# Optimization experiments

Measured on AMD Instinct MI355X. Metric: run time of the kernel, lower is better.

Reference implementation:

```python
import jax, jax.numpy as jnp
import numpy as np
from jax import lax

IMAGENET_MEAN = jnp.array([0.485, 0.456, 0.406], dtype=jnp.float32).reshape(1, 3, 1, 1)
IMAGENET_STD = jnp.array([0.229, 0.224, 0.225], dtype=jnp.float32).reshape(1, 3, 1, 1)
MAX_ITERS = 10
TEMPERATURE = 500.0


def conv3x3(x, w, b):
    # NCHW conv, stride 1, padding 1 (same as nn.Conv2d(k=3, padding=1))
    y = lax.conv_general_dilated(x, w, (1, 1), ((1, 1), (1, 1)),
                                 dimension_numbers=("NCHW", "OIHW", "NCHW"))
    return y + b[None, :, None, None]


def setup_inputs() -> dict:
    key = jax.random.key(0)
    k = jax.random.split(key, 8)
    B, H, W = 8, 512, 512
    real_img = jax.random.uniform(k[0], (B, 3, H, W), dtype=jnp.float32)
    pred_img = jax.random.uniform(k[1], (B, 3, H, W), dtype=jnp.float32)
    mask = jax.random.uniform(k[2], (B, 1, H, W), dtype=jnp.float32)
    # VGG19 first two convs (random-init stand-ins, scaled like kaiming-ish)
    w1 = jax.random.normal(k[3], (64, 3, 3, 3), dtype=jnp.float32) * 0.1
    b1 = jax.random.normal(k[4], (64,), dtype=jnp.float32) * 0.01
    w2 = jax.random.normal(k[5], (64, 64, 3, 3), dtype=jnp.float32) * 0.05
    b2 = jax.random.normal(k[6], (64,), dtype=jnp.float32) * 0.01
    erode_w = jnp.ones((1, 1, 3, 3), dtype=jnp.float32)  # weight.data.fill_(1)
    return {"real_img": real_img, "pred_img": pred_img, "mask": mask,
            "w1": w1, "b1": b1, "w2": w2, "b2": b2, "erode_w": erode_w}


def _forward(real_img, pred_img, mask, w1, b1, w2, b2, erode_w):
    x = (real_img - IMAGENET_MEAN) / IMAGENET_STD
    # features = conv1_1 -> relu -> conv1_2 -> relu (level=2, no pooling reached)
    f = jax.nn.relu(conv3x3(x, w1, b1))
    real_feats = jax.nn.relu(conv3x3(f, w2, b2))  # [B,64,H,W]

    dv = real_feats[:, :, 1:, :] - real_feats[:, :, :-1, :]
    vertical_sim = jnp.exp(-jnp.sum(dv * dv, axis=1, keepdims=True) / TEMPERATURE)  # [B,1,H-1,W]
    dh = real_feats[:, :, :, 1:] - real_feats[:, :, :, :-1]
    horizontal_sim = jnp.exp(-jnp.sum(dh * dh, axis=1, keepdims=True) / TEMPERATURE)  # [B,1,H,W-1]

    B, _, Hf, Wf = real_feats.shape
    # bilinear resize, half-pixel centers == F.interpolate(align_corners=False)
    mask_scaled = jax.image.resize(mask, (B, 1, Hf, Wf), method="bilinear")
    # erode: all-ones 3x3 conv (zero pad), threshold > 1
    eroded = lax.conv_general_dilated(mask_scaled, erode_w, (1, 1), ((1, 1), (1, 1)),
                                      dimension_numbers=("NCHW", "OIHW", "NCHW"))
    mask_scaled = (eroded > 1.0).astype(jnp.float32)

    cur0 = 1.0 - mask_scaled

    def body(i, cur):
        top = cur[:, :, :-1, :] * vertical_sim
        new_top = jnp.concatenate([top[:, :, :1, :], top], axis=2)  # replicate pad top
        bot = cur[:, :, 1:, :] * vertical_sim
        new_bot = jnp.concatenate([bot, bot[:, :, -1:, :]], axis=2)  # replicate pad bottom
        lef = cur[:, :, :, :-1] * horizontal_sim
        new_lef = jnp.concatenate([lef[:, :, :, :1], lef], axis=3)  # replicate pad left
        rig = cur[:, :, :, 1:] * horizontal_sim
        new_rig = jnp.concatenate([rig, rig[:, :, :, -1:]], axis=3)  # replicate pad right
        new_know = jnp.maximum(jnp.maximum(new_top, new_bot), jnp.maximum(new_lef, new_rig))
        return jnp.maximum(cur, new_know)

    cur_knowness = lax.fori_loop(0, MAX_ITERS, body, cur0)

    Hm, Wm = mask.shape[-2:]
    cur_knowness = jax.image.resize(cur_knowness, (B, 1, Hm, Wm), method="bilinear")
    return jnp.minimum(mask, 1.0 - cur_knowness)


def reference(real_img, pred_img, mask, w1, b1, w2, b2, erode_w):
    return _forward(real_img, pred_img, mask, w1, b1, w2, b2, erode_w)
```

## Files before the change

kernel.cpp:

```cpp
#include <hip/hip_runtime.h>
#include <hip/hip_bf16.h>

#define HH 512
#define WW 512
#define NB 8
#define IMG (HH*WW)
#define TS 15
#define NTL 35

typedef __bf16 bf16x8 __attribute__((ext_vector_type(8)));
typedef float  f32x4  __attribute__((ext_vector_type(4)));

__device__ __forceinline__ float bflo(unsigned u){ return __uint_as_float(u << 16); }
__device__ __forceinline__ float bfhi(unsigned u){ return __uint_as_float(u & 0xffff0000u); }
__device__ __forceinline__ unsigned f2bf_bits(float f){
    union { float f; unsigned u; } v; v.f = f;
    return (v.u + 0x7fffu + ((v.u >> 16) & 1u)) >> 16;
}
__device__ __forceinline__ unsigned packbf(float lo, float hi){
    return f2bf_bits(lo) | (f2bf_bits(hi) << 16);
}

__global__ void prep_kernel(const float* __restrict__ w2, const float* __restrict__ w1,
                            uint4* __restrict__ wb, uint4* __restrict__ wa)
{
    int i = blockIdx.x * 256 + threadIdx.x;
    if (i < 9*2*4*64){
        int tap = i >> 9;
        int rem = i & 511;
        int ks  = rem >> 8;
        int nf  = (rem >> 6) & 3;
        int l   = rem & 63;
        int oc  = nf*16 + (l & 15);
        int icb = ks*32 + (l >> 4)*8;
        float v[8];
        #pragma unroll
        for (int j = 0; j < 8; ++j)
            v[j] = w2[(oc*64 + icb + j)*9 + tap];
        uint4 q;
        q.x = packbf(v[0], v[1]); q.y = packbf(v[2], v[3]);
        q.z = packbf(v[4], v[5]); q.w = packbf(v[6], v[7]);
        wb[i] = q;
    } else if (i < 9*2*4*64 + 4*64){
        int idx = i - 9*2*4*64;
        int mf = idx >> 6, l = idx & 63;
        int oc = mf*16 + (l & 15);
        int kb = (l >> 4)*8;
        float v[8];
        #pragma unroll
        for (int j = 0; j < 8; ++j)
            v[j] = (kb + j < 27) ? w1[oc*27 + kb + j] : 0.f;
        uint4 q;
        q.x = packbf(v[0], v[1]); q.y = packbf(v[2], v[3]);
        q.z = packbf(v[4], v[5]); q.w = packbf(v[6], v[7]);
        wa[idx] = q;
    }
}

__global__ void erode_init_kernel(const float* __restrict__ mask, float* __restrict__ cur)
{
    int idx = blockIdx.x * 256 + threadIdx.x;
    int b = idx >> 18, r = idx & (IMG - 1);
    int h = r >> 9, w = r & 511;
    const float* mb = mask + b*IMG;
    float s = 0.f;
    #pragma unroll
    for (int dy = -1; dy <= 1; ++dy){
        int hh = h + dy;
        if (hh < 0 || hh >= HH) continue;
        #pragma unroll
        for (int dx = -1; dx <= 1; ++dx){
            int ww = w + dx;
            if (ww < 0 || ww >= WW) continue;
            s += mb[hh*WW + ww];
        }
    }
    cur[idx] = (s > 1.0f) ? 0.f : 1.f;
}

__global__ __launch_bounds__(256, 2)
void conv_sims_kernel(const float* __restrict__ img,
                      const float* __restrict__ b1,
                      const uint4* __restrict__ wa,
                      const uint4* __restrict__ wb, const float* __restrict__ b2,
                      float* __restrict__ vs, float* __restrict__ hs)
{
    __shared__ float xs[3][20][20];
    __shared__ uint4 fs4[324*8];
    __shared__ uint4 uni[2048];

    const int tid = threadIdx.x;
    const int bid = blockIdx.x;
    const int b   = bid / (NTL*NTL);
    const int t2  = bid % (NTL*NTL);
    const int th  = t2 / NTL, tw = t2 % NTL;
    const int h0  = th * TS, w0 = tw * TS;

    for (int i = tid; i < 3*20*20; i += 256){
        int ic = i / 400, r = (i / 20) % 20, c = i % 20;
        int gy = h0 - 2 + r, gx = w0 - 2 + c;
        float mean = (ic == 0) ? 0.485f : (ic == 1) ? 0.456f : 0.406f;
        float istd = (ic == 0) ? (1.f/0.229f) : (ic == 1) ? (1.f/0.224f) : (1.f/0.225f);
        float v = 0.f;
        if (gy >= 0 && gy < HH && gx >= 0 && gx < WW)
            v = (img[(b*3 + ic)*IMG + gy*WW + gx] - mean) * istd;
        xs[ic][r][c] = v;
    }
    __syncthreads();

    {
        uint4* xi = uni;
        for (int p = tid; p < 336; p += 256){
            uint4 c0 = {0,0,0,0}, c1 = c0, c2 = c0, c3 = c0;
            if (p < 324){
                int fy = p / 18, fx = p % 18;
                float xv[27];
                #pragma unroll
                for (int ic = 0; ic < 3; ++ic)
                    #pragma unroll
                    for (int ky = 0; ky < 3; ++ky)
                        #pragma unroll
                        for (int kx = 0; kx < 3; ++kx)
                            xv[ic*9 + ky*3 + kx] = xs[ic][fy + ky][fx + kx];
                c0.x = packbf(xv[0], xv[1]);  c0.y = packbf(xv[2], xv[3]);
                c0.z = packbf(xv[4], xv[5]);  c0.w = packbf(xv[6], xv[7]);
                c1.x = packbf(xv[8], xv[9]);  c1.y = packbf(xv[10], xv[11]);
                c1.z = packbf(xv[12], xv[13]);c1.w = packbf(xv[14], xv[15]);
                c2.x = packbf(xv[16], xv[17]);c2.y = packbf(xv[18], xv[19]);
                c2.z = packbf(xv[20], xv[21]);c2.w = packbf(xv[22], xv[23]);
                c3.x = packbf(xv[24], xv[25]);c3.y = packbf(xv[26], 0.f);
            }
            int sw = p & 3;
            xi[p*4 + (0 ^ sw)] = c0;
            xi[p*4 + (1 ^ sw)] = c1;
            xi[p*4 + (2 ^ sw)] = c2;
            xi[p*4 + (3 ^ sw)] = c3;
        }
    }
    __syncthreads();

    {
        const int l  = tid & 63, wv = tid >> 6;
        const int lr = l & 15,  kg = l >> 4;
        const bf16x8* wav = (const bf16x8*)wa;
        const bf16x8* xib = (const bf16x8*)uni;

        bf16x8 af[4];
        #pragma unroll
        for (int mf = 0; mf < 4; ++mf) af[mf] = wav[(mf << 6) + l];
        f32x4 binit[4];
        #pragma unroll
        for (int mf = 0; mf < 4; ++mf)
            binit[mf] = *(const f32x4*)(b1 + mf*16 + kg*4);

        for (int nb = wv; nb < 21; nb += 4){
            int px = nb*16 + lr;
            bf16x8 bf = xib[px*4 + (kg ^ (px & 3))];
            int fy = px / 18, fx = px % 18;
            int gy = h0 - 1 + fy, gx = w0 - 1 + fx;
            bool inimg = (px < 324) && gy >= 0 && gy < HH && gx >= 0 && gx < WW;
            #pragma unroll
            for (int mf = 0; mf < 4; ++mf){
                f32x4 acc = __builtin_amdgcn_mfma_f32_16x16x32_bf16(af[mf], bf, binit[mf], 0, 0, 0);
                unsigned lo = 0, hi = 0;
                if (inimg){
                    lo = packbf(fmaxf(acc[0], 0.f), fmaxf(acc[1], 0.f));
                    hi = packbf(fmaxf(acc[2], 0.f), fmaxf(acc[3], 0.f));
                }
                if (px < 324){
                    char* p8 = (char*)fs4 + px*128 + (((mf*2 + (kg >> 1)) ^ (px & 7)) << 4) + ((kg & 1) << 3);
                    uint2 w2v; w2v.x = lo; w2v.y = hi;
                    *(uint2*)p8 = w2v;
                }
            }
        }
    }
    __syncthreads();

    {
        const int wv = tid >> 6;
        const int l  = tid & 63;
        const int lr = l & 15;
        const int kg = l >> 4;

        f32x4 acc[4][4];
        #pragma unroll
        for (int nf = 0; nf < 4; ++nf){
            float bv = b2[nf*16 + lr];
            #pragma unroll
            for (int mf = 0; mf < 4; ++mf)
                acc[mf][nf] = (f32x4){bv, bv, bv, bv};
        }

        const bf16x8* fsb = (const bf16x8*)fs4;
        const bf16x8* wbv = (const bf16x8*)wb;

        #pragma unroll 1
        for (int tap = 0; tap < 9; ++tap){
            const int dy = tap / 3, dx = tap % 3;
            bf16x8 bfr[2][4];
            #pragma unroll
            for (int ks = 0; ks < 2; ++ks)
                #pragma unroll
                for (int nf = 0; nf < 4; ++nf)
                    bfr[ks][nf] = wbv[((tap*8 + ks*4 + nf) << 6) + l];
            #pragma unroll
            for (int ks = 0; ks < 2; ++ks){
                #pragma unroll
                for (int mf = 0; mf < 4; ++mf){
                    int fpx = (wv*4 + mf + dy)*18 + lr + dx;
                    bf16x8 afr = fsb[fpx*8 + ((ks*4 + kg) ^ (fpx & 7))];
                    #pragma unroll
                    for (int nf = 0; nf < 4; ++nf)
                        acc[mf][nf] = __builtin_amdgcn_mfma_f32_16x16x32_bf16(
                            afr, bfr[ks][nf], acc[mf][nf], 0, 0, 0);
                }
            }
        }

        unsigned short* ftu = (unsigned short*)uni;
        #pragma unroll
        for (int mf = 0; mf < 4; ++mf)
            #pragma unroll
            for (int nf = 0; nf < 4; ++nf)
                #pragma unroll
                for (int r = 0; r < 4; ++r){
                    int p  = wv*64 + mf*16 + kg*4 + r;
                    int oc = nf*16 + lr;
                    float v = fmaxf(acc[mf][nf][r], 0.f);
                    ftu[p*64 + (((oc >> 3) ^ (p & 7)) << 3) + (oc & 7)] =
                        (unsigned short)f2bf_bits(v);
                }
    }
    __syncthreads();

    const uint4* ft4 = uni;
    for (int s = tid; s < 450; s += 256){
        bool isv = (s < 225);
        int r  = isv ? s : (s - 225);
        int sy = r / 15, sx = r % 15;
        int gh = h0 + sy, gw = w0 + sx;
        if (gh >= HH || gw >= WW) continue;
        int pa = sy*16 + sx;
        int pb = isv ? (pa + 16) : (pa + 1);
        const uint4* A = ft4 + pa*8; int sa = pa & 7;
        const uint4* B = ft4 + pb*8; int sb = pb & 7;
        float ssd = 0.f;
        #pragma unroll
        for (int j = 0; j < 8; ++j){
            uint4 qa = A[j ^ sa], qb = B[j ^ sb];
            unsigned da[4] = {qa.x, qa.y, qa.z, qa.w};
            unsigned db[4] = {qb.x, qb.y, qb.z, qb.w};
            #pragma unroll
            for (int k = 0; k < 4; ++k){
                float d0 = bflo(da[k]) - bflo(db[k]);
                float d1 = bfhi(da[k]) - bfhi(db[k]);
                ssd = fmaf(d0, d0, ssd);
                ssd = fmaf(d1, d1, ssd);
            }
        }
        float sim = __expf(ssd * (-1.f/500.f));
        int o = b*IMG + gh*WW + gw;
        if (isv) vs[o] = (gh < HH-1) ? sim : 0.f;
        else     hs[o] = (gw < WW-1) ? sim : 0.f;
    }
}

template<bool FINAL>
__global__ __launch_bounds__(256, 2)
void prop5_kernel(const float* __restrict__ cin, float* __restrict__ cout,
                  const float* __restrict__ vs, const float* __restrict__ hs,
                  const float* __restrict__ mask, float* __restrict__ dout)
{
    __shared__ float cu[74*76];
    __shared__ float vl[74*76];
    __shared__ float hl[74*76];

    const int tid = threadIdx.x;
    const int bid = blockIdx.x;
    const int b  = bid >> 6;
    const int ty = (bid >> 3) & 7, tx = bid & 7;
    const int gy0 = ty*64 - 5, gx0 = tx*64 - 5;
    const float* cb = cin + b*IMG;
    const float* vb = vs  + b*IMG;
    const float* hb = hs  + b*IMG;

    for (int i = tid; i < 74*74; i += 256){
        int ly = i / 74, lx = i % 74;
        int gy = min(max(gy0 + ly, 0), 511);
        int gx = min(max(gx0 + lx, 0), 511);
        int g = gy*WW + gx, o = ly*76 + lx;
        cu[o] = cb[g];
        vl[o] = vb[g];
        hl[o] = hb[g];
    }
    __syncthreads();

    #pragma unroll
    for (int k = 1; k <= 5; ++k){
        const int S = 74 - 2*k;
        const int trips = (S*S + 255) / 256;
        float val[21];
        #pragma unroll
        for (int i = 0; i < trips; ++i){
            int px = tid + i*256;
            if (px < S*S){
                int y = px / S + k, x = px % S + k;
                int o = y*76 + x;
                float c  = cu[o];
                float tp = cu[o - 76] * vl[o - 76];
                float bt = cu[o + 76] * vl[o];
                float lf = cu[o - 1]  * hl[o - 1];
                float rg = cu[o + 1]  * hl[o];
                val[i] = fmaxf(fmaxf(c, fmaxf(tp, bt)), fmaxf(lf, rg));
            }
        }
        __syncthreads();
        #pragma unroll
        for (int i = 0; i < trips; ++i){
            int px = tid + i*256;
            if (px < S*S){
                int y = px / S + k, x = px % S + k;
                cu[y*76 + x] = val[i];
            }
        }
        __syncthreads();
    }

    const int gyc = ty*64, gxc = tx*64;
    for (int i = tid; i < 64*64; i += 256){
        int y = i >> 6, x = i & 63;
        float v = cu[(y + 5)*76 + (x + 5)];
        int g = b*IMG + (gyc + y)*WW + (gxc + x);
        if (FINAL) dout[g] = fminf(mask[g], 1.f - v);
        else       cout[g] = v;
    }
}

extern "C" void kernel_launch(void* const* d_in, const int* in_sizes, int n_in,
                              void* d_out, int out_size, void* d_ws, size_t ws_size,
                              hipStream_t stream)
{
    const float* img  = (const float*)d_in[0];
    const float* mask = (const float*)d_in[2];
    const float* w1   = (const float*)d_in[3];
    const float* b1   = (const float*)d_in[4];
    const float* w2   = (const float*)d_in[5];
    const float* b2   = (const float*)d_in[6];
    float* out = (float*)d_out;

    float* vs   = (float*)d_ws;
    float* hsm  = vs   + NB*IMG;
    float* curA = hsm  + NB*IMG;
    float* curB = curA + NB*IMG;
    uint4* wbuf = (uint4*)(curB + NB*IMG);
    uint4* wabuf = wbuf + 4608;

    prep_kernel<<<37, 256, 0, stream>>>(w2, w1, wbuf, wabuf);
    erode_init_kernel<<<NB*IMG/256, 256, 0, stream>>>(mask, curA);
    conv_sims_kernel<<<NB*NTL*NTL, 256, 0, stream>>>(img, b1, wabuf, wbuf, b2, vs, hsm);

    prop5_kernel<false><<<512, 256, 0, stream>>>(curA, curB, vs, hsm, mask, out);
    prop5_kernel<true ><<<512, 256, 0, stream>>>(curB, curB, vs, hsm, mask, out);
}
```

Measured before the change: 456.8 us.

## Fuse erosion into first propagation kernel and swap MFMA operand roles in conv2

```diff
diff --git a/kernel.cpp b/kernel.cpp
--- a/kernel.cpp
+++ b/kernel.cpp
@@ -55,27 +55,6 @@
         q.z = packbf(v[4], v[5]); q.w = packbf(v[6], v[7]);
         wa[idx] = q;
     }
-}
-
-__global__ void erode_init_kernel(const float* __restrict__ mask, float* __restrict__ cur)
-{
-    int idx = blockIdx.x * 256 + threadIdx.x;
-    int b = idx >> 18, r = idx & (IMG - 1);
-    int h = r >> 9, w = r & 511;
-    const float* mb = mask + b*IMG;
-    float s = 0.f;
-    #pragma unroll
-    for (int dy = -1; dy <= 1; ++dy){
-        int hh = h + dy;
-        if (hh < 0 || hh >= HH) continue;
-        #pragma unroll
-        for (int dx = -1; dx <= 1; ++dx){
-            int ww = w + dx;
-            if (ww < 0 || ww >= WW) continue;
-            s += mb[hh*WW + ww];
-        }
-    }
-    cur[idx] = (s > 1.0f) ? 0.f : 1.f;
 }
 
 __global__ __launch_bounds__(256, 2)
@@ -185,52 +164,50 @@
 
         f32x4 acc[4][4];
         #pragma unroll
-        for (int nf = 0; nf < 4; ++nf){
-            float bv = b2[nf*16 + lr];
-            #pragma unroll
-            for (int mf = 0; mf < 4; ++mf)
-                acc[mf][nf] = (f32x4){bv, bv, bv, bv};
+        for (int mf = 0; mf < 4; ++mf){
+            f32x4 bv = *(const f32x4*)(b2 + mf*16 + kg*4);
+            #pragma unroll
+            for (int nf = 0; nf < 4; ++nf) acc[mf][nf] = bv;
         }
 
         const bf16x8* fsb = (const bf16x8*)fs4;
         const bf16x8* wbv = (const bf16x8*)wb;
 
-        #pragma unroll 1
+        #pragma unroll
         for (int tap = 0; tap < 9; ++tap){
             const int dy = tap / 3, dx = tap % 3;
-            bf16x8 bfr[2][4];
-            #pragma unroll
-            for (int ks = 0; ks < 2; ++ks)
+            #pragma unroll
+            for (int ks = 0; ks < 2; ++ks){
+                bf16x8 wfr[4];
                 #pragma unroll
-                for (int nf = 0; nf < 4; ++nf)
-                    bfr[ks][nf] = wbv[((tap*8 + ks*4 + nf) << 6) + l];
-            #pragma unroll
-            for (int ks = 0; ks < 2; ++ks){
+                for (int mf = 0; mf < 4; ++mf)
+                    wfr[mf] = wbv[((tap*8 + ks*4 + mf) << 6) + l];
                 #pragma unroll
-                for (int mf = 0; mf < 4; ++mf){
-                    int fpx = (wv*4 + mf + dy)*18 + lr + dx;
-                    bf16x8 afr = fsb[fpx*8 + ((ks*4 + kg) ^ (fpx & 7))];
+                for (int nf = 0; nf < 4; ++nf){
+                    int fpx = (wv*4 + nf + dy)*18 + lr + dx;
+                    bf16x8 bfr = fsb[fpx*8 + ((ks*4 + kg) ^ (fpx & 7))];
                     #pragma unroll
-                    for (int nf = 0; nf < 4; ++nf)
+                    for (int mf = 0; mf < 4; ++mf)
                         acc[mf][nf] = __builtin_amdgcn_mfma_f32_16x16x32_bf16(
-                            afr, bfr[ks][nf], acc[mf][nf], 0, 0, 0);
+                            wfr[mf], bfr, acc[mf][nf], 0, 0, 0);
                 }
             }
         }
 
-        unsigned short* ftu = (unsigned short*)uni;
-        #pragma unroll
-        for (int mf = 0; mf < 4; ++mf)
-            #pragma unroll
-            for (int nf = 0; nf < 4; ++nf)
-                #pragma unroll
-                for (int r = 0; r < 4; ++r){
-                    int p  = wv*64 + mf*16 + kg*4 + r;
-                    int oc = nf*16 + lr;
-                    float v = fmaxf(acc[mf][nf][r], 0.f);
-                    ftu[p*64 + (((oc >> 3) ^ (p & 7)) << 3) + (oc & 7)] =
-                        (unsigned short)f2bf_bits(v);
-                }
+        char* ftb = (char*)uni;
+        #pragma unroll
+        for (int nf = 0; nf < 4; ++nf){
+            int px = wv*64 + nf*16 + lr;
+            char* pbase = ftb + px*128 + ((kg & 1) << 3);
+            int swz = px & 7;
+            #pragma unroll
+            for (int mf = 0; mf < 4; ++mf){
+                uint2 wv2;
+                wv2.x = packbf(fmaxf(acc[mf][nf][0], 0.f), fmaxf(acc[mf][nf][1], 0.f));
+                wv2.y = packbf(fmaxf(acc[mf][nf][2], 0.f), fmaxf(acc[mf][nf][3], 0.f));
+                *(uint2*)(pbase + (((mf*2 + (kg >> 1)) ^ swz) << 4)) = wv2;
+            }
+        }
     }
     __syncthreads();
 
@@ -266,13 +243,13 @@
     }
 }
 
-template<bool FINAL>
+template<bool FIRST, bool FINAL>
 __global__ __launch_bounds__(256, 2)
 void prop5_kernel(const float* __restrict__ cin, float* __restrict__ cout,
                   const float* __restrict__ vs, const float* __restrict__ hs,
                   const float* __restrict__ mask, float* __restrict__ dout)
 {
-    __shared__ float cu[74*76];
+    __shared__ float cu[76*78];
     __shared__ float vl[74*76];
     __shared__ float hl[74*76];
 
@@ -281,20 +258,73 @@
     const int b  = bid >> 6;
     const int ty = (bid >> 3) & 7, tx = bid & 7;
     const int gy0 = ty*64 - 5, gx0 = tx*64 - 5;
-    const float* cb = cin + b*IMG;
-    const float* vb = vs  + b*IMG;
-    const float* hb = hs  + b*IMG;
+    const float* vb = vs + b*IMG;
+    const float* hb = hs + b*IMG;
 
     for (int i = tid; i < 74*74; i += 256){
         int ly = i / 74, lx = i % 74;
         int gy = min(max(gy0 + ly, 0), 511);
         int gx = min(max(gx0 + lx, 0), 511);
         int g = gy*WW + gx, o = ly*76 + lx;
-        cu[o] = cb[g];
         vl[o] = vb[g];
         hl[o] = hb[g];
     }
-    __syncthreads();
+
+    if (FIRST){
+        const float* mb = mask + b*IMG;
+        for (int i = tid; i < 76*76; i += 256){
+            int ly = i / 76, lx = i % 76;
+            int gy = gy0 - 1 + ly, gx = gx0 - 1 + lx;
+            float v = 0.f;
+            if (gy >= 0 && gy < HH && gx >= 0 && gx < WW) v = mb[gy*WW + gx];
+            cu[ly*78 + lx] = v;
+        }
+        __syncthreads();
+        float val[22];
+        #pragma unroll
+        for (int i = 0; i < 22; ++i){
+            int px = tid + i*256;
+            if (px < 74*74){
+                int ly = px / 74, lx = px % 74;
+                int o = ly*78 + lx;
+                float s = cu[o]     + cu[o+1]   + cu[o+2]
+                        + cu[o+78]  + cu[o+79]  + cu[o+80]
+                        + cu[o+156] + cu[o+157] + cu[o+158];
+                val[i] = (s > 1.0f) ? 0.f : 1.f;
+            }
+        }
+        __syncthreads();
+        #pragma unroll
+        for (int i = 0; i < 22; ++i){
+            int px = tid + i*256;
+            if (px < 74*74){
+                int ly = px / 74, lx = px % 74;
+                int gy = gy0 + ly, gx = gx0 + lx;
+                if (gy >= 0 && gy < HH && gx >= 0 && gx < WW)
+                    cu[(ly+1)*78 + (lx+1)] = val[i];
+            }
+        }
+        __syncthreads();
+        for (int i = tid; i < 74*74; i += 256){
+            int ly = i / 74, lx = i % 74;
+            int gy = gy0 + ly, gx = gx0 + lx;
+            if (gy < 0 || gy >= HH || gx < 0 || gx >= WW){
+                int cly = min(max(gy, 0), 511) - gy0;
+                int clx = min(max(gx, 0), 511) - gx0;
+                cu[(ly+1)*78 + (lx+1)] = cu[(cly+1)*78 + (clx+1)];
+            }
+        }
+        __syncthreads();
+    } else {
+        const float* cb = cin + b*IMG;
+        for (int i = tid; i < 74*74; i += 256){
+            int ly = i / 74, lx = i % 74;
+            int gy = min(max(gy0 + ly, 0), 511);
+            int gx = min(max(gx0 + lx, 0), 511);
+            cu[(ly+1)*78 + (lx+1)] = cb[gy*WW + gx];
+        }
+        __syncthreads();
+    }
 
     #pragma unroll
     for (int k = 1; k <= 5; ++k){
@@ -306,12 +336,13 @@
             int px = tid + i*256;
             if (px < S*S){
                 int y = px / S + k, x = px % S + k;
-                int o = y*76 + x;
-                float c  = cu[o];
-                float tp = cu[o - 76] * vl[o - 76];
-                float bt = cu[o + 76] * vl[o];
-                float lf = cu[o - 1]  * hl[o - 1];
-                float rg = cu[o + 1]  * hl[o];
+                int oc_ = (y + 1)*78 + (x + 1);
+                int os  = y*76 + x;
+                float c  = cu[oc_];
+                float tp = cu[oc_ - 78] * vl[os - 76];
+                float bt = cu[oc_ + 78] * vl[os];
+                float lf = cu[oc_ - 1]  * hl[os - 1];
+                float rg = cu[oc_ + 1]  * hl[os];
                 val[i] = fmaxf(fmaxf(c, fmaxf(tp, bt)), fmaxf(lf, rg));
             }
         }
@@ -321,7 +352,7 @@
             int px = tid + i*256;
             if (px < S*S){
                 int y = px / S + k, x = px % S + k;
-                cu[y*76 + x] = val[i];
+                cu[(y + 1)*78 + (x + 1)] = val[i];
             }
         }
         __syncthreads();
@@ -330,7 +361,7 @@
     const int gyc = ty*64, gxc = tx*64;
     for (int i = tid; i < 64*64; i += 256){
         int y = i >> 6, x = i & 63;
-        float v = cu[(y + 5)*76 + (x + 5)];
+        float v = cu[(y + 6)*78 + (x + 6)];
         int g = b*IMG + (gyc + y)*WW + (gxc + x);
         if (FINAL) dout[g] = fminf(mask[g], 1.f - v);
         else       cout[g] = v;
@@ -351,15 +382,13 @@
 
     float* vs   = (float*)d_ws;
     float* hsm  = vs   + NB*IMG;
-    float* curA = hsm  + NB*IMG;
-    float* curB = curA + NB*IMG;
+    float* curB = hsm  + NB*IMG;
     uint4* wbuf = (uint4*)(curB + NB*IMG);
     uint4* wabuf = wbuf + 4608;
 
     prep_kernel<<<37, 256, 0, stream>>>(w2, w1, wbuf, wabuf);
-    erode_init_kernel<<<NB*IMG/256, 256, 0, stream>>>(mask, curA);
     conv_sims_kernel<<<NB*NTL*NTL, 256, 0, stream>>>(img, b1, wabuf, wbuf, b2, vs, hsm);
 
-    prop5_kernel<false><<<512, 256, 0, stream>>>(curA, curB, vs, hsm, mask, out);
-    prop5_kernel<true ><<<512, 256, 0, stream>>>(curB, curB, vs, hsm, mask, out);
-}
+    prop5_kernel<true,  false><<<512, 256, 0, stream>>>(curB, curB, vs, hsm, mask, out);
+    prop5_kernel<false, true ><<<512, 256, 0, stream>>>(curB, curB, vs, hsm, mask, out);
+}
```

Measured after the change: 444.4 us. 1.03x faster.
